# Performance work log

Hardware: AMD Instinct MI355X
Metric: run time of the kernel (lower is better)

Reference implementation:

```python
import jax, jax.numpy as jnp
import numpy as np

EMBED = 1024
D_FF = 4 * EMBED
N_EXPERTS = 8
TOP_K = 2
B, S = 2, 1024


def setup_inputs() -> dict:
    key = jax.random.key(0)
    ks = jax.random.split(key, 10)
    sc_d = 1.0 / np.sqrt(EMBED)
    sc_h = 1.0 / np.sqrt(D_FF)
    return {
        "inputs": jax.random.normal(ks[0], (B, S, EMBED), jnp.float32),
        # router MLP: Linear(D,4D) -> ReLU -> Linear(4D,E)
        "rw1": jax.random.normal(ks[1], (EMBED, D_FF), jnp.float32) * sc_d,
        "rb1": jnp.zeros((D_FF,), jnp.float32),
        "rw2": jax.random.normal(ks[2], (D_FF, N_EXPERTS), jnp.float32) * sc_h,
        "rb2": jnp.zeros((N_EXPERTS,), jnp.float32),
        # stacked expert weights: Linear(D,4D) -> ReLU -> Linear(4D,D)
        "W1": jax.random.normal(ks[3], (N_EXPERTS, EMBED, D_FF), jnp.float32) * sc_d,
        "b1": jnp.zeros((N_EXPERTS, D_FF), jnp.float32),
        "W2": jax.random.normal(ks[4], (N_EXPERTS, D_FF, EMBED), jnp.float32) * sc_h,
        "b2": jnp.zeros((N_EXPERTS, EMBED), jnp.float32),
    }


def reference(inputs, rw1, rb1, rw2, rb2, W1, b1, W2, b2):
    Bb, Ss, D = inputs.shape
    T = Bb * Ss
    xf = inputs.reshape(T, D)  # [T, D]

    # Router: scores over experts, keep top-k, softmax over kept entries only.
    score = jax.nn.relu(xf @ rw1 + rb1) @ rw2 + rb2          # [T, E]
    _, topi = jax.lax.top_k(score, TOP_K)                    # [T, K]
    mask = jnp.zeros(score.shape, bool).at[jnp.arange(T)[:, None], topi].set(True)
    gate = jax.nn.softmax(jnp.where(mask, score, -jnp.inf), axis=-1)  # [T, E]

    # Dense per-expert MLP weighted by gate; gate==0 for non-top-k experts,
    # matching the original masked gather/scatter exactly.
    out = jnp.zeros_like(xf)
    for e in range(N_EXPERTS):
        h = jax.nn.relu(xf @ W1[e] + b1[e])                  # [T, 4D]
        y = h @ W2[e] + b2[e]                                # [T, D]
        out = out + gate[:, e:e + 1] * y
    return out.reshape(Bb, Ss, D)
```

## Files before the change

### kernel.cpp

```cpp
#include <hip/hip_runtime.h>
#include <stdint.h>

typedef unsigned short ushort_t;
typedef __attribute__((ext_vector_type(8))) short short8;
typedef __attribute__((ext_vector_type(4))) float f32x4;

#define EMBED   1024
#define DFF     4096
#define NEXP    8
#define TOKENS  2048
#define SLOTS   4096
#define TMAX    40
#define TG      ((TMAX + 7) / 8)

__device__ __forceinline__ ushort_t f2bf(float f) {
  unsigned u = __float_as_uint(f);
  u += 0x7FFFu + ((u >> 16) & 1u);
  return (ushort_t)(u >> 16);
}
__device__ __forceinline__ float bf2f(ushort_t b) {
  return __uint_as_float(((unsigned)b) << 16);
}

__device__ __forceinline__ void gl2lds16(const void* g, void* l) {
  typedef const __attribute__((address_space(1))) unsigned char* gp_t;
  typedef __attribute__((address_space(3))) unsigned char* lp_t;
  __builtin_amdgcn_global_load_lds((gp_t)(uintptr_t)g, (lp_t)(uintptr_t)l, 16, 0, 0);
}

__global__ void zero_small(int* counts, int* cursors) {
  int i = threadIdx.x;
  if (i < NEXP) { counts[i] = 0; cursors[i] = 0; }
}

__global__ void split_xhl(const float* __restrict__ x, ushort_t* __restrict__ Xs) {
  int t = blockIdx.x;
  int d = threadIdx.x * 4;
  float4 v = *(const float4*)(x + (size_t)t * EMBED + d);
  ushort4 hi, lo;
  hi.x = f2bf(v.x); lo.x = f2bf(v.x - bf2f(hi.x));
  hi.y = f2bf(v.y); lo.y = f2bf(v.y - bf2f(hi.y));
  hi.z = f2bf(v.z); lo.z = f2bf(v.z - bf2f(hi.z));
  hi.w = f2bf(v.w); lo.w = f2bf(v.w - bf2f(hi.w));
  ushort_t* row = Xs + (size_t)t * 2048;
  *(ushort4*)(row + d)        = hi;
  *(ushort4*)(row + 1024 + d) = lo;
}

__global__ void transp_conv(const float* __restrict__ src, ushort_t* __restrict__ dst,
                            int src_ld, int dst_ld, long src_estride, long dst_estride,
                            int dst_koff, int lo)
{
  __shared__ float t[64][65];
  const float* s = src + (size_t)blockIdx.z * src_estride;
  ushort_t* d = dst + (size_t)blockIdx.z * dst_estride;
  int n0 = blockIdx.x * 64, k0 = blockIdx.y * 64;
  int tid = threadIdx.x;
  int kk = tid >> 4, nn = (tid & 15) * 4;
  #pragma unroll
  for (int it = 0; it < 4; it++) {
    float4 v = *(const float4*)(s + (size_t)(k0 + kk + it * 16) * src_ld + n0 + nn);
    t[kk + it * 16][nn]     = v.x;
    t[kk + it * 16][nn + 1] = v.y;
    t[kk + it * 16][nn + 2] = v.z;
    t[kk + it * 16][nn + 3] = v.w;
  }
  __syncthreads();
  int nn2 = tid >> 3, kk2 = (tid & 7) * 8;
  #pragma unroll
  for (int it = 0; it < 2; it++) {
    int n = nn2 + it * 32;
    union { ushort_t u[8]; uint4 v; } pk;
    #pragma unroll
    for (int j = 0; j < 8; j++) {
      float xv = t[kk2 + j][n];
      ushort_t hv = f2bf(xv);
      pk.u[j] = lo ? f2bf(xv - bf2f(hv)) : hv;
    }
    *(uint4*)(d + (size_t)(n0 + n) * dst_ld + dst_koff + k0 + kk2) = pk.v;
  }
}

template<int APATH, int OUTMODE, bool RELU, bool EXPERT, int SPLITK, int NX>
__global__ __launch_bounds__(256, 3)
void gemm_kernel(const ushort_t* __restrict__ A, const ushort_t* __restrict__ B,
                 const float* __restrict__ bias, void* __restrict__ Cout,
                 const float* __restrict__ slot_gate, const int* __restrict__ slot_token,
                 const int* __restrict__ off, const int* __restrict__ tile_e,
                 const int* __restrict__ tile_y, int e0, int e1,
                 int M, int N, int K)
{
  __shared__ ushort_t As[3][128 * 32];
  __shared__ ushort_t Bs[3][128 * 32];

  int e = 0, kc = 0, row0, col0, m_base, m_cnt;
  if (EXPERT) {
    constexpr int INNER = NX * SPLITK;
    int bid = blockIdx.x;
    int xcd = bid & 7;
    int j   = bid >> 3;
    int t   = xcd + 8 * (j / INNER);
    int i   = j % INNER;
    int xi  = i % NX;
    kc      = i / NX;
    e = tile_e[t];
    if (e < e0 || e >= e1) return;
    row0   = tile_y[t] * 128;
    col0   = xi * 128;
    m_base = off[e];
    m_cnt  = off[e + 1] - m_base;
  } else {
    row0 = blockIdx.y * 128;
    col0 = blockIdx.x * 128;
    m_base = 0; m_cnt = M;
    if (row0 >= m_cnt) return;
  }
  const int Kc   = K / SPLITK;
  const int kbeg = kc * Kc;

  const int tid  = threadIdx.x;
  const int lane = tid & 63;
  const int wid  = tid >> 6;
  const int wm = wid & 1, wn = wid >> 1;

  const int srow  = lane >> 2;
  const int schk8 = ((lane & 3) ^ ((lane >> 3) & 3)) * 8;

  const ushort_t* gA[2];
  const ushort_t* gB[2];
  int aoff[2];
  const ushort_t* Bt = B + (EXPERT ? (size_t)(e - e0) * (size_t)N * K : 0);
  #pragma unroll
  for (int h = 0; h < 2; h++) {
    int r  = row0 + h * 64 + wid * 16 + srow;
    int rl = min(r, m_cnt - 1);
    size_t rowb;
    if (APATH == 2)      rowb = (size_t)slot_token[m_base + rl] * 2048;
    else if (APATH == 1) rowb = (size_t)rl * 2048;
    else                 rowb = (size_t)(m_base + rl) * (size_t)K;
    gA[h]   = A + rowb + (APATH == 0 ? kbeg : 0) + schk8;
    aoff[h] = (h * 64 + wid * 16) * 32;

    int n = col0 + h * 64 + wid * 16 + srow;
    gB[h] = Bt + (size_t)n * K + kbeg + schk8;
  }

  auto stage = [&](int pb, int kt) {
    const int k0 = kt << 5;
    const int k0a = (APATH == 1 && k0 >= 2048) ? k0 - 2048 : k0;
    #pragma unroll
    for (int h = 0; h < 2; h++) {
      gl2lds16(gA[h] + k0a, &As[pb][aoff[h]]);
      gl2lds16(gB[h] + k0,  &Bs[pb][aoff[h]]);
    }
  };

  f32x4 acc[4][4];
  #pragma unroll
  for (int i = 0; i < 4; i++)
    #pragma unroll
    for (int j = 0; j < 4; j++)
      acc[i][j] = (f32x4){0.f, 0.f, 0.f, 0.f};

  const int q  = lane >> 4;
  const int rr = lane & 15;
  const int sw8 = (q ^ ((rr >> 1) & 3)) * 8;
  const int abase = (wm * 64 + rr) * 32 + sw8;
  const int bbase = (wn * 64 + rr) * 32 + sw8;

  const int nkt = Kc >> 5;

  stage(0, 0);
  if (nkt > 1) stage(1, 1);

  for (int kt = 0; kt < nkt; kt++) {
    if (kt + 1 < nkt) asm volatile("s_waitcnt vmcnt(4)" ::: "memory");
    else              asm volatile("s_waitcnt vmcnt(0)" ::: "memory");
    __builtin_amdgcn_s_barrier();
    __builtin_amdgcn_sched_barrier(0);
    if (kt + 2 < nkt) stage((kt + 2) % 3, kt + 2);

    const int cur = kt % 3;
    short8 af[4], bfr[4];
    #pragma unroll
    for (int i = 0; i < 4; i++) {
      af[i]  = *(const short8*)(&As[cur][abase + i * 512]);
      bfr[i] = *(const short8*)(&Bs[cur][bbase + i * 512]);
    }
    asm volatile("s_waitcnt lgkmcnt(0)" ::: "memory");
    __builtin_amdgcn_sched_barrier(0);
    #pragma unroll
    for (int mt = 0; mt < 4; mt++)
      #pragma unroll
      for (int nt = 0; nt < 4; nt++)
        acc[mt][nt] = __builtin_amdgcn_mfma_f32_16x16x32_bf16(af[mt], bfr[nt], acc[mt][nt], 0, 0, 0);
  }

  const float* biasp = bias + (EXPERT ? (size_t)e * N : 0);
  float bv[4];
  #pragma unroll
  for (int nt = 0; nt < 4; nt++)
    bv[nt] = biasp[col0 + wn * 64 + nt * 16 + rr];
  const float bscale = (SPLITK == 1 || kc == 0) ? 1.f : 0.f;

  if constexpr (OUTMODE == 4) {
    const float* rw2p = slot_gate;
    float4 wa[4], wb[4];
    #pragma unroll
    for (int nt = 0; nt < 4; nt++) {
      int c = col0 + wn * 64 + nt * 16 + rr;
      wa[nt] = *(const float4*)(rw2p + (size_t)c * 8);
      wb[nt] = *(const float4*)(rw2p + (size_t)c * 8 + 4);
    }
    float* Ps = (float*)Cout;
    const int xi2 = (col0 >> 6) + wn;
    #pragma unroll
    for (int mt = 0; mt < 4; mt++) {
      #pragma unroll
      for (int i = 0; i < 4; i++) {
        float4 sA = {0.f, 0.f, 0.f, 0.f}, sB = {0.f, 0.f, 0.f, 0.f};
        #pragma unroll
        for (int nt = 0; nt < 4; nt++) {
          float v = acc[mt][nt][i] + bv[nt];
          if (RELU) v = fmaxf(v, 0.f);
          sA.x += v * wa[nt].x; sA.y += v * wa[nt].y;
          sA.z += v * wa[nt].z; sA.w += v * wa[nt].w;
          sB.x += v * wb[nt].x; sB.y += v * wb[nt].y;
          sB.z += v * wb[nt].z; sB.w += v * wb[nt].w;
        }
        #pragma unroll
        for (int o = 1; o <= 8; o <<= 1) {
          sA.x += __shfl_xor(sA.x, o); sA.y += __shfl_xor(sA.y, o);
          sA.z += __shfl_xor(sA.z, o); sA.w += __shfl_xor(sA.w, o);
          sB.x += __shfl_xor(sB.x, o); sB.y += __shfl_xor(sB.y, o);
          sB.z += __shfl_xor(sB.z, o); sB.w += __shfl_xor(sB.w, o);
        }
        if (rr == 0) {
          int row = row0 + wm * 64 + mt * 16 + q * 4 + i;
          float* p = Ps + ((size_t)row * 64 + xi2) * 8;
          *(float4*)p       = sA;
          *(float4*)(p + 4) = sB;
        }
      }
    }
  } else {
    #pragma unroll
    for (int mt = 0; mt < 4; mt++) {
      #pragma unroll
      for (int i = 0; i < 4; i++) {
        int r_loc = row0 + wm * 64 + mt * 16 + q * 4 + i;
        if (r_loc < m_cnt) {
          int slot = m_base + r_loc;
          float g = 1.f;
          if (OUTMODE == 3) g = slot_gate[slot];
          #pragma unroll
          for (int nt = 0; nt < 4; nt++) {
            float v = acc[mt][nt][i] + bscale * bv[nt];
            if (RELU) v = fmaxf(v, 0.f);
            int c = col0 + wn * 64 + nt * 16 + rr;
            if (OUTMODE == 0)      ((float*)Cout)[(size_t)slot * N + c]    = v;
            else if (OUTMODE == 1) ((ushort_t*)Cout)[(size_t)slot * N + c] = f2bf(v);
            else ((float*)Cout)[((size_t)kc * SLOTS + slot) * N + c] = g * v;
          }
        }
      }
    }
  }
}

__global__ void router_reduce(const float* __restrict__ Ps, const float* __restrict__ rb2,
                              int* __restrict__ topi, float* __restrict__ gates,
                              int* __restrict__ counts)
{
  int t = blockIdx.x * 4 + (threadIdx.x >> 6);
  if (t >= TOKENS) return;
  int lane = threadIdx.x & 63;
  const float* pt = Ps + (size_t)t * 512;
  float4 v0 = *(const float4*)(pt + lane * 8);
  float4 v1 = *(const float4*)(pt + lane * 8 + 4);
  #pragma unroll
  for (int o = 1; o <= 32; o <<= 1) {
    v0.x += __shfl_xor(v0.x, o); v0.y += __shfl_xor(v0.y, o);
    v0.z += __shfl_xor(v0.z, o); v0.w += __shfl_xor(v0.w, o);
    v1.x += __shfl_xor(v1.x, o); v1.y += __shfl_xor(v1.y, o);
    v1.z += __shfl_xor(v1.z, o); v1.w += __shfl_xor(v1.w, o);
  }
  if (lane == 0) {
    float s[8] = {v0.x + rb2[0], v0.y + rb2[1], v0.z + rb2[2], v0.w + rb2[3],
                  v1.x + rb2[4], v1.y + rb2[5], v1.z + rb2[6], v1.w + rb2[7]};
    int i0 = 0;
    #pragma unroll
    for (int e = 1; e < 8; e++) if (s[e] > s[i0]) i0 = e;
    int i1 = (i0 == 0) ? 1 : 0;
    #pragma unroll
    for (int e = 0; e < 8; e++) if (e != i0 && s[e] > s[i1]) i1 = e;
    float ex = __expf(s[i1] - s[i0]);
    float g0 = 1.f / (1.f + ex);
    float g1 = ex / (1.f + ex);
    topi[t * 2] = i0; topi[t * 2 + 1] = i1;
    gates[t * 2] = g0; gates[t * 2 + 1] = g1;
    atomicAdd(&counts[i0], 1);
    atomicAdd(&counts[i1], 1);
  }
}

__global__ void prefix_off(const int* __restrict__ counts, int* __restrict__ off,
                           int* __restrict__ tile_e, int* __restrict__ tile_y)
{
  if (threadIdx.x == 0) {
    int a = 0, t = 0;
    for (int e = 0; e < NEXP; e++) {
      off[e] = a;
      int c = counts[e]; a += c;
      int ty = (c + 127) >> 7;
      for (int y = 0; y < ty; y++) { tile_e[t] = e; tile_y[t] = y; t++; }
    }
    off[NEXP] = a;
    for (; t < TMAX; t++) { tile_e[t] = -1; tile_y[t] = 0; }
  }
}

__global__ void assign_slots(const int* __restrict__ topi, const float* __restrict__ gates,
                             const int* __restrict__ off, int* __restrict__ cursors,
                             int* __restrict__ slot_token, float* __restrict__ slot_gate,
                             int* __restrict__ tok_slot)
{
  int t = blockIdx.x * blockDim.x + threadIdx.x;
  if (t >= TOKENS) return;
  #pragma unroll
  for (int k = 0; k < 2; k++) {
    int e = topi[t * 2 + k];
    int p = atomicAdd(&cursors[e], 1);
    int s = off[e] + p;
    slot_token[s] = t;
    slot_gate[s]  = gates[t * 2 + k];
    tok_slot[t * 2 + k] = s;
  }
}

template<int NC>
__global__ void combine_out(const float* __restrict__ Ys, const int* __restrict__ tok_slot,
                            float* __restrict__ out)
{
  int t = blockIdx.x;
  int d = threadIdx.x * 4;
  int s0 = tok_slot[t * 2], s1 = tok_slot[t * 2 + 1];
  float4 o = {0.f, 0.f, 0.f, 0.f};
  #pragma unroll
  for (int k = 0; k < NC; k++) {
    float4 a = *(const float4*)(Ys + ((size_t)k * SLOTS + s0) * EMBED + d);
    float4 b = *(const float4*)(Ys + ((size_t)k * SLOTS + s1) * EMBED + d);
    o.x += a.x + b.x;
    o.y += a.y + b.y;
    o.z += a.z + b.z;
    o.w += a.w + b.w;
  }
  *(float4*)(out + (size_t)t * EMBED + d) = o;
}

extern "C" void kernel_launch(void* const* d_in, const int* in_sizes, int n_in,
                              void* d_out, int out_size, void* d_ws, size_t ws_size,
                              hipStream_t stream)
{
  const float* x   = (const float*)d_in[0];
  const float* rw1 = (const float*)d_in[1];
  const float* rb1 = (const float*)d_in[2];
  const float* rw2 = (const float*)d_in[3];
  const float* rb2 = (const float*)d_in[4];
  const float* W1  = (const float*)d_in[5];
  const float* b1  = (const float*)d_in[6];
  const float* W2  = (const float*)d_in[7];
  const float* b2  = (const float*)d_in[8];
  float* out = (float*)d_out;
  char* ws = (char*)d_ws;

  const long W1ES = (long)EMBED * DFF;
  const long W2ES = (long)DFF * EMBED;
  const size_t SZ_R = (size_t)4096 * 4096 * 2;

  const bool FULL = ws_size >= ((size_t)300 << 20);

  if (FULL) {
    char* p = ws;
    ushort_t* W1T  = (ushort_t*)p;  p += (size_t)NEXP * DFF * EMBED * 2;
    ushort_t* W2T  = (ushort_t*)p;  p += (size_t)NEXP * EMBED * DFF * 2;
    ushort_t* RW1t = (ushort_t*)p;  p += (size_t)4096 * 3072 * 2;
    ushort_t* Hs   = (ushort_t*)p;  p += (size_t)SLOTS * DFF * 2;
    ushort_t* Xhl  = (ushort_t*)p;  p += (size_t)TOKENS * 2048 * 2;
    float*    Ys   = (float*)p;     p += (size_t)4 * SLOTS * EMBED * 4;
    float*    Ps   = (float*)p;     p += (size_t)TOKENS * 512 * 4;
    int*   topi       = (int*)p;    p += TOKENS * 2 * 4;
    float* gates      = (float*)p;  p += TOKENS * 2 * 4;
    int*   tok_slot   = (int*)p;    p += TOKENS * 2 * 4;
    int*   slot_token = (int*)p;    p += SLOTS * 4;
    float* slot_gate  = (float*)p;  p += SLOTS * 4;
    int*   counts     = (int*)p;    p += 256;
    int*   cursors    = (int*)p;    p += 256;
    int*   off        = (int*)p;    p += 256;
    int*   tile_e     = (int*)p;    p += 256;
    int*   tile_y     = (int*)p;    p += 256;

    zero_small<<<1, 64, 0, stream>>>(counts, cursors);
    split_xhl<<<TOKENS, 256, 0, stream>>>(x, Xhl);

    transp_conv<<<dim3(64, 16, 1), 256, 0, stream>>>(rw1, RW1t, DFF, 3072, 0, 0, 0,    0);
    transp_conv<<<dim3(64, 16, 1), 256, 0, stream>>>(rw1, RW1t, DFF, 3072, 0, 0, 1024, 0);
    transp_conv<<<dim3(64, 16, 1), 256, 0, stream>>>(rw1, RW1t, DFF, 3072, 0, 0, 2048, 1);

    gemm_kernel<1, 4, true, false, 1, 32>
        <<<dim3(32, 16, 1), 256, 0, stream>>>(Xhl, RW1t, rb1, Ps, rw2, nullptr,
                                              nullptr, nullptr, nullptr, 0, NEXP,
                                              TOKENS, DFF, 3072);
    router_reduce<<<512, 256, 0, stream>>>(Ps, rb2, topi, gates, counts);
    prefix_off  <<<1, 64, 0, stream>>>(counts, off, tile_e, tile_y);
    assign_slots<<<8, 256, 0, stream>>>(topi, gates, off, cursors, slot_token, slot_gate, tok_slot);

    transp_conv<<<dim3(64, 16, 8), 256, 0, stream>>>(W1, W1T, DFF, EMBED, W1ES, W1ES, 0, 0);
    gemm_kernel<2, 1, true, true, 1, 32>
        <<<dim3(8 * TG * 32, 1, 1), 256, 0, stream>>>(Xhl, W1T, b1, Hs,
            nullptr, slot_token, off, tile_e, tile_y, 0, NEXP, 0, DFF, EMBED);

    transp_conv<<<dim3(16, 64, 8), 256, 0, stream>>>(W2, W2T, EMBED, DFF, W2ES, W2ES, 0, 0);
    gemm_kernel<0, 3, false, true, 4, 8>
        <<<dim3(8 * TG * 32, 1, 1), 256, 0, stream>>>(Hs, W2T, b2, Ys,
            slot_gate, nullptr, off, tile_e, tile_y, 0, NEXP, 0, EMBED, DFF);

    combine_out<4><<<TOKENS, 256, 0, stream>>>(Ys, tok_slot, out);
  } else {
    ushort_t* RW1t = (ushort_t*)ws;
    ushort_t* WT   = (ushort_t*)ws;
    ushort_t* Hs   = (ushort_t*)(ws + SZ_R);
    ushort_t* Xhl  = (ushort_t*)(ws + 2 * SZ_R);
    float*    Ys   = (float*)(ws + 2 * SZ_R);
    char* p = ws + 3 * SZ_R;
    float* Ps         = (float*)p;  p += (size_t)TOKENS * 512 * 4;
    int*   topi       = (int*)p;    p += TOKENS * 2 * 4;
    float* gates      = (float*)p;  p += TOKENS * 2 * 4;
    int*   tok_slot   = (int*)p;    p += TOKENS * 2 * 4;
    int*   slot_token = (int*)p;    p += SLOTS * 4;
    float* slot_gate  = (float*)p;  p += SLOTS * 4;
    int*   counts     = (int*)p;    p += 256;
    int*   cursors    = (int*)p;    p += 256;
    int*   off        = (int*)p;    p += 256;
    int*   tile_e     = (int*)p;    p += 256;
    int*   tile_y     = (int*)p;    p += 256;

    zero_small<<<1, 64, 0, stream>>>(counts, cursors);
    split_xhl<<<TOKENS, 256, 0, stream>>>(x, Xhl);

    transp_conv<<<dim3(64, 16, 1), 256, 0, stream>>>(rw1, RW1t, DFF, 3072, 0, 0, 0,    0);
    transp_conv<<<dim3(64, 16, 1), 256, 0, stream>>>(rw1, RW1t, DFF, 3072, 0, 0, 1024, 0);
    transp_conv<<<dim3(64, 16, 1), 256, 0, stream>>>(rw1, RW1t, DFF, 3072, 0, 0, 2048, 1);

    gemm_kernel<1, 4, true, false, 1, 32>
        <<<dim3(32, 16, 1), 256, 0, stream>>>(Xhl, RW1t, rb1, Ps, rw2, nullptr,
                                              nullptr, nullptr, nullptr, 0, NEXP,
                                              TOKENS, DFF, 3072);
    router_reduce<<<512, 256, 0, stream>>>(Ps, rb2, topi, gates, counts);
    prefix_off  <<<1, 64, 0, stream>>>(counts, off, tile_e, tile_y);
    assign_slots<<<8, 256, 0, stream>>>(topi, gates, off, cursors, slot_token, slot_gate, tok_slot);

    for (int half = 0; half < 2; half++) {
      int e0 = half * 4;
      transp_conv<<<dim3(64, 16, 4), 256, 0, stream>>>(W1 + (size_t)e0 * W1ES, WT,
          DFF, EMBED, W1ES, W1ES, 0, 0);
      gemm_kernel<2, 1, true, true, 1, 32>
          <<<dim3(8 * TG * 32, 1, 1), 256, 0, stream>>>(Xhl, WT, b1, Hs,
              nullptr, slot_token, off, tile_e, tile_y, e0, e0 + 4, 0, DFF, EMBED);
    }
    for (int half = 0; half < 2; half++) {
      int e0 = half * 4;
      transp_conv<<<dim3(16, 64, 4), 256, 0, stream>>>(W2 + (size_t)e0 * W2ES, WT,
          EMBED, DFF, W2ES, W2ES, 0, 0);
      gemm_kernel<0, 3, false, true, 2, 8>
          <<<dim3(8 * TG * 16, 1, 1), 256, 0, stream>>>(Hs, WT, b2, Ys,
              slot_gate, nullptr, off, tile_e, tile_y, e0, e0 + 4, 0, EMBED, DFF);
    }

    combine_out<2><<<TOKENS, 256, 0, stream>>>(Ys, tok_slot, out);
  }
}
```

Before: 617.3 us.

## Fuse expert weight transposes into router GEMM launch and merge small kernels

Merges the input bf16 split, the counts zeroing and the three router-weight transposes into one prep kernel. The W1/W2 expert weight transposes become extra blocks appended to the router GEMM grid, so they run alongside it instead of as separate serialized launches. The prefix and slot-assignment kernels become a single one-block kernel that uses shared-memory cursors. This cuts launch count and lets the bandwidth-bound weight conversion overlap compute-bound GEMM work. The cost is a single-block assignment loop and a larger, heterogeneous grid that may interfere with router GEMM scheduling.

```diff
diff --git a/kernel.cpp b/kernel.cpp
--- a/kernel.cpp
+++ b/kernel.cpp
@@ -28,38 +28,17 @@
   __builtin_amdgcn_global_load_lds((gp_t)(uintptr_t)g, (lp_t)(uintptr_t)l, 16, 0, 0);
 }
 
-__global__ void zero_small(int* counts, int* cursors) {
-  int i = threadIdx.x;
-  if (i < NEXP) { counts[i] = 0; cursors[i] = 0; }
-}
-
-__global__ void split_xhl(const float* __restrict__ x, ushort_t* __restrict__ Xs) {
-  int t = blockIdx.x;
-  int d = threadIdx.x * 4;
-  float4 v = *(const float4*)(x + (size_t)t * EMBED + d);
-  ushort4 hi, lo;
-  hi.x = f2bf(v.x); lo.x = f2bf(v.x - bf2f(hi.x));
-  hi.y = f2bf(v.y); lo.y = f2bf(v.y - bf2f(hi.y));
-  hi.z = f2bf(v.z); lo.z = f2bf(v.z - bf2f(hi.z));
-  hi.w = f2bf(v.w); lo.w = f2bf(v.w - bf2f(hi.w));
-  ushort_t* row = Xs + (size_t)t * 2048;
-  *(ushort4*)(row + d)        = hi;
-  *(ushort4*)(row + 1024 + d) = lo;
-}
-
-__global__ void transp_conv(const float* __restrict__ src, ushort_t* __restrict__ dst,
-                            int src_ld, int dst_ld, long src_estride, long dst_estride,
-                            int dst_koff, int lo)
-{
-  __shared__ float t[64][65];
-  const float* s = src + (size_t)blockIdx.z * src_estride;
-  ushort_t* d = dst + (size_t)blockIdx.z * dst_estride;
-  int n0 = blockIdx.x * 64, k0 = blockIdx.y * 64;
+__device__ __forceinline__ void transp_body(const float* __restrict__ src,
+                                            ushort_t* __restrict__ dst,
+                                            int src_ld, int dst_ld, int bx, int by,
+                                            int dst_koff, int lo, float (*t)[65])
+{
+  int n0 = bx * 64, k0 = by * 64;
   int tid = threadIdx.x;
   int kk = tid >> 4, nn = (tid & 15) * 4;
   #pragma unroll
   for (int it = 0; it < 4; it++) {
-    float4 v = *(const float4*)(s + (size_t)(k0 + kk + it * 16) * src_ld + n0 + nn);
+    float4 v = *(const float4*)(src + (size_t)(k0 + kk + it * 16) * src_ld + n0 + nn);
     t[kk + it * 16][nn]     = v.x;
     t[kk + it * 16][nn + 1] = v.y;
     t[kk + it * 16][nn + 2] = v.z;
@@ -77,21 +56,77 @@
       ushort_t hv = f2bf(xv);
       pk.u[j] = lo ? f2bf(xv - bf2f(hv)) : hv;
     }
-    *(uint4*)(d + (size_t)(n0 + n) * dst_ld + dst_koff + k0 + kk2) = pk.v;
-  }
-}
-
-template<int APATH, int OUTMODE, bool RELU, bool EXPERT, int SPLITK, int NX>
+    *(uint4*)(dst + (size_t)(n0 + n) * dst_ld + dst_koff + k0 + kk2) = pk.v;
+  }
+}
+
+__global__ void transp_conv(const float* __restrict__ src, ushort_t* __restrict__ dst,
+                            int src_ld, int dst_ld, long src_estride, long dst_estride,
+                            int dst_koff, int lo)
+{
+  __shared__ __align__(16) float t[64][65];
+  transp_body(src + (size_t)blockIdx.z * src_estride,
+              dst + (size_t)blockIdx.z * dst_estride,
+              src_ld, dst_ld, blockIdx.x, blockIdx.y, dst_koff, lo, t);
+}
+
+__global__ __launch_bounds__(256) void prep_kernel(const float* __restrict__ x,
+    ushort_t* __restrict__ Xs, const float* __restrict__ rw1,
+    ushort_t* __restrict__ RW1t, int* __restrict__ counts)
+{
+  __shared__ __align__(16) float tt[64][65];
+  int bid = blockIdx.x;
+  if (bid < TOKENS) {
+    if (bid == 0 && threadIdx.x < NEXP) counts[threadIdx.x] = 0;
+    int d = threadIdx.x * 4;
+    float4 v = *(const float4*)(x + (size_t)bid * EMBED + d);
+    ushort4 hi, lo;
+    hi.x = f2bf(v.x); lo.x = f2bf(v.x - bf2f(hi.x));
+    hi.y = f2bf(v.y); lo.y = f2bf(v.y - bf2f(hi.y));
+    hi.z = f2bf(v.z); lo.z = f2bf(v.z - bf2f(hi.z));
+    hi.w = f2bf(v.w); lo.w = f2bf(v.w - bf2f(hi.w));
+    ushort_t* row = Xs + (size_t)bid * 2048;
+    *(ushort4*)(row + d)        = hi;
+    *(ushort4*)(row + 1024 + d) = lo;
+    return;
+  }
+  int idx = bid - TOKENS;
+  int which = idx >> 10, sub = idx & 1023;
+  transp_body(rw1, RW1t, DFF, 3072, sub & 63, sub >> 6, which * 1024, which == 2, tt);
+}
+
+template<int APATH, int OUTMODE, bool RELU, bool EXPERT, int SPLITK, int NX, int NFUSE>
 __global__ __launch_bounds__(256, 3)
 void gemm_kernel(const ushort_t* __restrict__ A, const ushort_t* __restrict__ B,
                  const float* __restrict__ bias, void* __restrict__ Cout,
                  const float* __restrict__ slot_gate, const int* __restrict__ slot_token,
                  const int* __restrict__ off, const int* __restrict__ tile_e,
                  const int* __restrict__ tile_y, int e0, int e1,
-                 int M, int N, int K)
-{
-  __shared__ ushort_t As[3][128 * 32];
-  __shared__ ushort_t Bs[3][128 * 32];
+                 int M, int N, int K, int ngb,
+                 const float* __restrict__ tsrc0, ushort_t* __restrict__ tdst0,
+                 const float* __restrict__ tsrc1, ushort_t* __restrict__ tdst1)
+{
+  __shared__ __align__(16) char lds_raw[49152];
+  auto As = (ushort_t(*)[4096])lds_raw;
+  auto Bs = (ushort_t(*)[4096])(lds_raw + 24576);
+
+  if constexpr (NFUSE > 0) {
+    int bidf = blockIdx.x;
+    if (bidf >= ngb) {
+      int idx = bidf - ngb;
+      auto tt = (float(*)[65])lds_raw;
+      const size_t ES = (size_t)EMBED * DFF;
+      if (idx < 64 * 16 * 8) {
+        int bx = idx & 63, by = (idx >> 6) & 15, z = idx >> 10;
+        transp_body(tsrc0 + z * ES, tdst0 + z * ES, DFF, EMBED, bx, by, 0, 0, tt);
+      } else {
+        idx -= 64 * 16 * 8;
+        int bx = idx & 15, by = (idx >> 4) & 63, z = idx >> 10;
+        transp_body(tsrc1 + z * ES, tdst1 + z * ES, EMBED, DFF, bx, by, 0, 0, tt);
+      }
+      return;
+    }
+  }
 
   int e = 0, kc = 0, row0, col0, m_base, m_cnt;
   if (EXPERT) {
@@ -110,8 +145,9 @@
     m_base = off[e];
     m_cnt  = off[e + 1] - m_base;
   } else {
-    row0 = blockIdx.y * 128;
-    col0 = blockIdx.x * 128;
+    int bid = blockIdx.x;
+    row0 = (bid >> 5) * 128;
+    col0 = (bid & 31) * 128;
     m_base = 0; m_cnt = M;
     if (row0 >= m_cnt) return;
   }
@@ -304,13 +340,20 @@
   }
 }
 
-__global__ void prefix_off(const int* __restrict__ counts, int* __restrict__ off,
-                           int* __restrict__ tile_e, int* __restrict__ tile_y)
-{
-  if (threadIdx.x == 0) {
+__global__ void assign_all(const int* __restrict__ counts, const int* __restrict__ topi,
+                           const float* __restrict__ gates, int* __restrict__ off,
+                           int* __restrict__ tile_e, int* __restrict__ tile_y,
+                           int* __restrict__ slot_token, float* __restrict__ slot_gate,
+                           int* __restrict__ tok_slot)
+{
+  __shared__ int s_off[NEXP];
+  __shared__ int s_cur[NEXP];
+  int tid = threadIdx.x;
+  if (tid < NEXP) s_cur[tid] = 0;
+  if (tid == 0) {
     int a = 0, t = 0;
     for (int e = 0; e < NEXP; e++) {
-      off[e] = a;
+      off[e] = a; s_off[e] = a;
       int c = counts[e]; a += c;
       int ty = (c + 127) >> 7;
       for (int y = 0; y < ty; y++) { tile_e[t] = e; tile_y[t] = y; t++; }
@@ -318,23 +361,17 @@
     off[NEXP] = a;
     for (; t < TMAX; t++) { tile_e[t] = -1; tile_y[t] = 0; }
   }
-}
-
-__global__ void assign_slots(const int* __restrict__ topi, const float* __restrict__ gates,
-                             const int* __restrict__ off, int* __restrict__ cursors,
-                             int* __restrict__ slot_token, float* __restrict__ slot_gate,
-                             int* __restrict__ tok_slot)
-{
-  int t = blockIdx.x * blockDim.x + threadIdx.x;
-  if (t >= TOKENS) return;
-  #pragma unroll
-  for (int k = 0; k < 2; k++) {
-    int e = topi[t * 2 + k];
-    int p = atomicAdd(&cursors[e], 1);
-    int s = off[e] + p;
-    slot_token[s] = t;
-    slot_gate[s]  = gates[t * 2 + k];
-    tok_slot[t * 2 + k] = s;
+  __syncthreads();
+  for (int t = tid; t < TOKENS; t += 256) {
+    #pragma unroll
+    for (int k = 0; k < 2; k++) {
+      int e = topi[t * 2 + k];
+      int p = atomicAdd(&s_cur[e], 1);
+      int s = s_off[e] + p;
+      slot_token[s] = t;
+      slot_gate[s]  = gates[t * 2 + k];
+      tok_slot[t * 2 + k] = s;
+    }
   }
 }
 
@@ -395,35 +432,30 @@
     int*   slot_token = (int*)p;    p += SLOTS * 4;
     float* slot_gate  = (float*)p;  p += SLOTS * 4;
     int*   counts     = (int*)p;    p += 256;
-    int*   cursors    = (int*)p;    p += 256;
     int*   off        = (int*)p;    p += 256;
     int*   tile_e     = (int*)p;    p += 256;
     int*   tile_y     = (int*)p;    p += 256;
 
-    zero_small<<<1, 64, 0, stream>>>(counts, cursors);
-    split_xhl<<<TOKENS, 256, 0, stream>>>(x, Xhl);
-
-    transp_conv<<<dim3(64, 16, 1), 256, 0, stream>>>(rw1, RW1t, DFF, 3072, 0, 0, 0,    0);
-    transp_conv<<<dim3(64, 16, 1), 256, 0, stream>>>(rw1, RW1t, DFF, 3072, 0, 0, 1024, 0);
-    transp_conv<<<dim3(64, 16, 1), 256, 0, stream>>>(rw1, RW1t, DFF, 3072, 0, 0, 2048, 1);
-
-    gemm_kernel<1, 4, true, false, 1, 32>
-        <<<dim3(32, 16, 1), 256, 0, stream>>>(Xhl, RW1t, rb1, Ps, rw2, nullptr,
-                                              nullptr, nullptr, nullptr, 0, NEXP,
-                                              TOKENS, DFF, 3072);
+    prep_kernel<<<TOKENS + 3 * 1024, 256, 0, stream>>>(x, Xhl, rw1, RW1t, counts);
+
+    gemm_kernel<1, 4, true, false, 1, 32, 2>
+        <<<dim3(512 + 16384, 1, 1), 256, 0, stream>>>(Xhl, RW1t, rb1, Ps, rw2,
+            nullptr, nullptr, nullptr, nullptr, 0, NEXP, TOKENS, DFF, 3072,
+            512, W1, W1T, W2, W2T);
+
     router_reduce<<<512, 256, 0, stream>>>(Ps, rb2, topi, gates, counts);
-    prefix_off  <<<1, 64, 0, stream>>>(counts, off, tile_e, tile_y);
-    assign_slots<<<8, 256, 0, stream>>>(topi, gates, off, cursors, slot_token, slot_gate, tok_slot);
-
-    transp_conv<<<dim3(64, 16, 8), 256, 0, stream>>>(W1, W1T, DFF, EMBED, W1ES, W1ES, 0, 0);
-    gemm_kernel<2, 1, true, true, 1, 32>
+    assign_all<<<1, 256, 0, stream>>>(counts, topi, gates, off, tile_e, tile_y,
+                                      slot_token, slot_gate, tok_slot);
+
+    gemm_kernel<2, 1, true, true, 1, 32, 0>
         <<<dim3(8 * TG * 32, 1, 1), 256, 0, stream>>>(Xhl, W1T, b1, Hs,
-            nullptr, slot_token, off, tile_e, tile_y, 0, NEXP, 0, DFF, EMBED);
-
-    transp_conv<<<dim3(16, 64, 8), 256, 0, stream>>>(W2, W2T, EMBED, DFF, W2ES, W2ES, 0, 0);
-    gemm_kernel<0, 3, false, true, 4, 8>
+            nullptr, slot_token, off, tile_e, tile_y, 0, NEXP, 0, DFF, EMBED,
+            0, nullptr, nullptr, nullptr, nullptr);
+
+    gemm_kernel<0, 3, false, true, 4, 8, 0>
         <<<dim3(8 * TG * 32, 1, 1), 256, 0, stream>>>(Hs, W2T, b2, Ys,
-            slot_gate, nullptr, off, tile_e, tile_y, 0, NEXP, 0, EMBED, DFF);
+            slot_gate, nullptr, off, tile_e, tile_y, 0, NEXP, 0, EMBED, DFF,
+            0, nullptr, nullptr, nullptr, nullptr);
 
     combine_out<4><<<TOKENS, 256, 0, stream>>>(Ys, tok_slot, out);
   } else {
@@ -440,41 +472,37 @@
     int*   slot_token = (int*)p;    p += SLOTS * 4;
     float* slot_gate  = (float*)p;  p += SLOTS * 4;
     int*   counts     = (int*)p;    p += 256;
-    int*   cursors    = (int*)p;    p += 256;
     int*   off        = (int*)p;    p += 256;
     int*   tile_e     = (int*)p;    p += 256;
     int*   tile_y     = (int*)p;    p += 256;
 
-    zero_small<<<1, 64, 0, stream>>>(counts, cursors);
-    split_xhl<<<TOKENS, 256, 0, stream>>>(x, Xhl);
-
-    transp_conv<<<dim3(64, 16, 1), 256, 0, stream>>>(rw1, RW1t, DFF, 3072, 0, 0, 0,    0);
-    transp_conv<<<dim3(64, 16, 1), 256, 0, stream>>>(rw1, RW1t, DFF, 3072, 0, 0, 1024, 0);
-    transp_conv<<<dim3(64, 16, 1), 256, 0, stream>>>(rw1, RW1t, DFF, 3072, 0, 0, 2048, 1);
-
-    gemm_kernel<1, 4, true, false, 1, 32>
-        <<<dim3(32, 16, 1), 256, 0, stream>>>(Xhl, RW1t, rb1, Ps, rw2, nullptr,
-                                              nullptr, nullptr, nullptr, 0, NEXP,
-                                              TOKENS, DFF, 3072);
+    prep_kernel<<<TOKENS + 3 * 1024, 256, 0, stream>>>(x, Xhl, rw1, RW1t, counts);
+
+    gemm_kernel<1, 4, true, false, 1, 32, 0>
+        <<<dim3(512, 1, 1), 256, 0, stream>>>(Xhl, RW1t, rb1, Ps, rw2, nullptr,
+            nullptr, nullptr, nullptr, 0, NEXP, TOKENS, DFF, 3072,
+            0, nullptr, nullptr, nullptr, nullptr);
     router_reduce<<<512, 256, 0, stream>>>(Ps, rb2, topi, gates, counts);
-    prefix_off  <<<1, 64, 0, stream>>>(counts, off, tile_e, tile_y);
-    assign_slots<<<8, 256, 0, stream>>>(topi, gates, off, cursors, slot_token, slot_gate, tok_slot);
+    assign_all<<<1, 256, 0, stream>>>(counts, topi, gates, off, tile_e, tile_y,
+                                      slot_token, slot_gate, tok_slot);
 
     for (int half = 0; half < 2; half++) {
       int e0 = half * 4;
       transp_conv<<<dim3(64, 16, 4), 256, 0, stream>>>(W1 + (size_t)e0 * W1ES, WT,
           DFF, EMBED, W1ES, W1ES, 0, 0);
-      gemm_kernel<2, 1, true, true, 1, 32>
+      gemm_kernel<2, 1, true, true, 1, 32, 0>
           <<<dim3(8 * TG * 32, 1, 1), 256, 0, stream>>>(Xhl, WT, b1, Hs,
-              nullptr, slot_token, off, tile_e, tile_y, e0, e0 + 4, 0, DFF, EMBED);
+              nullptr, slot_token, off, tile_e, tile_y, e0, e0 + 4, 0, DFF, EMBED,
+              0, nullptr, nullptr, nullptr, nullptr);
     }
     for (int half = 0; half < 2; half++) {
       int e0 = half * 4;
       transp_conv<<<dim3(16, 64, 4), 256, 0, stream>>>(W2 + (size_t)e0 * W2ES, WT,
           EMBED, DFF, W2ES, W2ES, 0, 0);
-      gemm_kernel<0, 3, false, true, 2, 8>
+      gemm_kernel<0, 3, false, true, 2, 8, 0>
           <<<dim3(8 * TG * 16, 1, 1), 256, 0, stream>>>(Hs, WT, b2, Ys,
-              slot_gate, nullptr, off, tile_e, tile_y, e0, e0 + 4, 0, EMBED, DFF);
+              slot_gate, nullptr, off, tile_e, tile_y, e0, e0 + 4, 0, EMBED, DFF,
+              0, nullptr, nullptr, nullptr, nullptr);
     }
 
     combine_out<2><<<TOKENS, 256, 0, stream>>>(Ys, tok_slot, out);
```

Result: faster. 564.1 us (-8.6%).
